# Kernel tuning notes

Hardware: AMD Instinct MI355X
Metric: run time of the kernel (lower is better)

The kernel has to match this reference:

```python
import jax, jax.numpy as jnp
import numpy as np

B = 32        # number of graphs
NPG = 2048    # nodes per graph (equal sizes -> max_size == NPG)
N = B * NPG   # total nodes
DEG = 16      # average degree
E = N * DEG   # total edges
F_IN = 128    # num_node_feats
LATENT = [32, 32, 32, 1]
TOTAL = sum(LATENT)  # 97
K = 30        # phi output size (DGCNN k)
OUT = 32      # output_dim


def setup_inputs() -> dict:
    key = jax.random.key(0)
    ks = jax.random.split(key, 16)
    node_feat = jax.random.normal(ks[0], (N, F_IN), jnp.float32)

    # edges constrained within each graph (block-diagonal n2n adjacency)
    rng = np.random.default_rng(0)
    offsets = np.repeat(np.arange(B, dtype=np.int64) * NPG, NPG * DEG)
    src = rng.integers(0, NPG, size=E) + offsets
    dst = rng.integers(0, NPG, size=E) + offsets
    edge_index = jnp.asarray(np.stack([src, dst]).astype(np.int32))

    # node_degs = in-degree + 1, shape [N, 1]
    degs = np.bincount(dst, minlength=N).astype(np.float32)
    node_degs = jnp.asarray(degs + 1.0)[:, None]

    def lin(k, fan_in, fan_out):
        s = 1.0 / np.sqrt(fan_in)
        kw, kb = jax.random.split(k)
        W = jax.random.uniform(kw, (fan_in, fan_out), jnp.float32, -s, s)
        b = jax.random.uniform(kb, (fan_out,), jnp.float32, -s, s)
        return W, b

    dims = [F_IN] + LATENT
    params = {}
    for i in range(len(LATENT)):
        W, b = lin(ks[1 + i], dims[i], dims[i + 1])
        params[f"W{i}"] = W
        params[f"b{i}"] = b
    params["phi_W"], params["phi_b"] = lin(ks[10], TOTAL, K)
    params["rho_W"], params["rho_b"] = lin(ks[11], K, OUT)

    return dict(node_feat=node_feat, node_degs=node_degs, edge_index=edge_index, **params)


def reference(node_feat, node_degs, W0, b0, W1, b1, W2, b2, W3, b3,
              phi_W, phi_b, rho_W, rho_b, edge_index):
    src, dst = edge_index[0], edge_index[1]
    n = node_feat.shape[0]

    def spmm(x):  # n2n adjacency @ x via gather + segment-sum
        return jax.ops.segment_sum(x[src], dst, num_segments=n)

    h = node_feat
    layers = [(W0, b0), (W1, b1), (W2, b2), (W3, b3)]
    cats = []
    for W, b in layers:
        pooled = spmm(h) + h                       # A h + h
        h = jnp.tanh((pooled @ W + b) / node_degs)  # linear, degree norm, tanh
        cats.append(h)
    msg = jnp.concatenate(cats, axis=1)            # [N, 97]

    # sortpooling-to-batched tensor: equal graph sizes -> pure reshape
    batched = msg.reshape(B, NPG, TOTAL)

    # DeepSets invariant model: rho(sum_i phi(x_i))
    phi = jax.nn.relu(batched @ phi_W + phi_b)     # [B, NPG, K]
    summed = jnp.sum(phi, axis=1)                  # [B, K]
    out = summed @ rho_W + rho_b                   # [B, OUT]
    return out
```

## Files before the change

### kernel.cpp

```cpp
#include <hip/hip_runtime.h>
#include <hip/hip_bf16.h>

#define NN 65536
#define NE (NN * 16)
#define NG 32
#define MAXD 64

#define WS_CURSOR 0
#define WS_SUMMED 262144
#define WS_ELL    1048576
#define WS_ZA     (WS_ELL + NN * MAXD * 4)
#define WS_ZB     (WS_ZA + NN * 32 * 4)
#define WS_H1     (WS_ZB + NN * 32 * 4)
#define WS_H2     (WS_H1 + NN * 32 * 4)
#define WS_H3     (WS_H2 + NN * 32 * 4)
#define WS_Z4     (WS_H3 + NN * 32 * 4)

__device__ __forceinline__ int xcd_swz(int b, int chunk) {
    return (b & 7) * chunk + (b >> 3);
}

__global__ __launch_bounds__(256) void k_build(const int* __restrict__ ei,
                                               int* __restrict__ cursor,
                                               int* __restrict__ ell) {
    int blk = xcd_swz(blockIdx.x, NE / 1024 / 8);
    int idx = blk * 256 + threadIdx.x;
    const int4* e4 = (const int4*)ei;
    int4 s = e4[idx];
    int4 d = e4[NE / 4 + idx];
    int t;
    t = atomicAdd(&cursor[d.x], 1); if (t < MAXD) ell[d.x * MAXD + t] = s.x;
    t = atomicAdd(&cursor[d.y], 1); if (t < MAXD) ell[d.y * MAXD + t] = s.y;
    t = atomicAdd(&cursor[d.z], 1); if (t < MAXD) ell[d.z * MAXD + t] = s.z;
    t = atomicAdd(&cursor[d.w], 1); if (t < MAXD) ell[d.w * MAXD + t] = s.w;
}

__global__ __launch_bounds__(256) void k_gemm1(const float* __restrict__ feat,
                                               const float* __restrict__ W0,
                                               float* __restrict__ z1) {
    __shared__ float wl[32 * 132];
    __shared__ float hl[64 * 132];
    int tid = threadIdx.x;
    for (int i = tid; i < 128 * 32; i += 256) {
        int k = i >> 5, c = i & 31;
        wl[c * 132 + k] = W0[i];
    }
    int base = blockIdx.x * 64;
    const float* fsrc = feat + (size_t)base * 128;
    #pragma unroll
    for (int v = 0; v < 8; ++v) {
        int flat = v * 1024 + tid * 4;
        int rr = flat >> 7, kk = flat & 127;
        *(float4*)&hl[rr * 132 + kk] = *(const float4*)&fsrc[flat];
    }
    __syncthreads();
    int cg = tid & 15, rg = tid >> 4;
    int c0 = cg * 2, r0 = rg * 4;
    float acc[4][2] = {};
    #pragma unroll 2
    for (int k = 0; k < 128; k += 4) {
        float4 wa = *(const float4*)&wl[c0 * 132 + k];
        float4 wb = *(const float4*)&wl[(c0 + 1) * 132 + k];
        #pragma unroll
        for (int rr = 0; rr < 4; ++rr) {
            float4 hv = *(const float4*)&hl[(r0 + rr) * 132 + k];
            acc[rr][0] += hv.x * wa.x + hv.y * wa.y + hv.z * wa.z + hv.w * wa.w;
            acc[rr][1] += hv.x * wb.x + hv.y * wb.y + hv.z * wb.z + hv.w * wb.w;
        }
    }
    #pragma unroll
    for (int rr = 0; rr < 4; ++rr) {
        int d = base + r0 + rr;
        z1[d * 32 + c0]     = acc[rr][0];
        z1[d * 32 + c0 + 1] = acc[rr][1];
    }
}

__device__ __forceinline__ float gather32(const int* __restrict__ row, int cnt,
                                          const float* __restrict__ zin, int c) {
    int i0 = row[c];
    float acc = 0.f;
    int m = cnt < 32 ? cnt : 32;
    int j = 0;
    for (; j + 8 <= m; j += 8) {
        int s0 = __shfl(i0, j, 32),     s1 = __shfl(i0, j + 1, 32);
        int s2 = __shfl(i0, j + 2, 32), s3 = __shfl(i0, j + 3, 32);
        int s4 = __shfl(i0, j + 4, 32), s5 = __shfl(i0, j + 5, 32);
        int s6 = __shfl(i0, j + 6, 32), s7 = __shfl(i0, j + 7, 32);
        float t0 = zin[s0 * 32 + c], t1 = zin[s1 * 32 + c];
        float t2 = zin[s2 * 32 + c], t3 = zin[s3 * 32 + c];
        float t4 = zin[s4 * 32 + c], t5 = zin[s5 * 32 + c];
        float t6 = zin[s6 * 32 + c], t7 = zin[s7 * 32 + c];
        acc += ((t0 + t1) + (t2 + t3)) + ((t4 + t5) + (t6 + t7));
    }
    for (; j + 2 <= m; j += 2) {
        int s0 = __shfl(i0, j, 32), s1 = __shfl(i0, j + 1, 32);
        float t0 = zin[s0 * 32 + c], t1 = zin[s1 * 32 + c];
        acc += t0 + t1;
    }
    for (; j < m; ++j) acc += zin[__shfl(i0, j, 32) * 32 + c];
    if (cnt > 32) {
        int i1 = row[32 + c];
        for (int j2 = 32; j2 < cnt; ++j2)
            acc += zin[__shfl(i1, j2 - 32, 32) * 32 + c];
    }
    return acc;
}

__global__ __launch_bounds__(256) void k_layer(const int* __restrict__ cursor,
                                               const int* __restrict__ ell,
                                               const float* __restrict__ zin,
                                               const float* __restrict__ degs,
                                               const float* __restrict__ bias,
                                               const float* __restrict__ Wn,
                                               float* __restrict__ hout,
                                               float* __restrict__ znext) {
    __shared__ float wt[32 * 36];
    __shared__ float hl[8][36];
    int tid = threadIdx.x;
    for (int i = tid; i < 1024; i += 256) {
        int k = i >> 5, c = i & 31;
        wt[c * 36 + k] = Wn[i];
    }
    int blk = xcd_swz(blockIdx.x, NN / 8 / 8);
    int r = tid >> 5, c = tid & 31;
    int d = blk * 8 + r;
    int cnt = cursor[d]; if (cnt > MAXD) cnt = MAXD;
    const int* row = ell + (size_t)d * MAXD;
    float acc = gather32(row, cnt, zin, c);
    float val = tanhf((acc + zin[d * 32 + c] + bias[c]) / degs[d]);
    hout[d * 32 + c] = val;
    hl[r][c] = val;
    __syncthreads();
    const float* hrow = &hl[r][0];
    const float* wrow = wt + c * 36;
    float4 a4 = {0.f, 0.f, 0.f, 0.f};
    #pragma unroll
    for (int k = 0; k < 32; k += 4) {
        float4 hv = *(const float4*)&hrow[k];
        float4 wv = *(const float4*)&wrow[k];
        a4.x += hv.x * wv.x; a4.y += hv.y * wv.y;
        a4.z += hv.z * wv.z; a4.w += hv.w * wv.w;
    }
    znext[d * 32 + c] = (a4.x + a4.y) + (a4.z + a4.w);
}

__global__ __launch_bounds__(256) void k_layer3(const int* __restrict__ cursor,
                                                const int* __restrict__ ell,
                                                const float* __restrict__ zin,
                                                const float* __restrict__ degs,
                                                const float* __restrict__ bias,
                                                const float* __restrict__ W3,
                                                float* __restrict__ hout,
                                                float* __restrict__ z4) {
    int tid = threadIdx.x;
    int blk = xcd_swz(blockIdx.x, NN / 8 / 8);
    int r = tid >> 5, c = tid & 31;
    int d = blk * 8 + r;
    int cnt = cursor[d]; if (cnt > MAXD) cnt = MAXD;
    const int* row = ell + (size_t)d * MAXD;
    float acc = gather32(row, cnt, zin, c);
    float val = tanhf((acc + zin[d * 32 + c] + bias[c]) / degs[d]);
    hout[d * 32 + c] = val;
    float v = val * W3[c];
    #pragma unroll
    for (int off = 16; off; off >>= 1) v += __shfl_xor(v, off, 32);
    if (c == 0) z4[d] = v;
}

__global__ __launch_bounds__(256) void k_phi(const int* __restrict__ cursor,
                                             const int* __restrict__ ell,
                                             const float* __restrict__ z4,
                                             const float* __restrict__ degs,
                                             const float* __restrict__ b3,
                                             const float* __restrict__ h1,
                                             const float* __restrict__ h2,
                                             const float* __restrict__ h3,
                                             const float* __restrict__ phiW,
                                             const float* __restrict__ phib,
                                             float* __restrict__ summed) {
    __shared__ float pl[30 * 100];
    __shared__ float ml[8 * 100];
    __shared__ float part[4][32];
    int tid = threadIdx.x;
    for (int i = tid; i < 30 * 97; i += 256) {
        int cc = i / 97, jj = i - cc * 97;
        pl[cc * 100 + jj] = phiW[jj * 30 + cc];
    }
    int blk = xcd_swz(blockIdx.x, NN / 8 / 8);
    int r = tid >> 5, c = tid & 31;
    int d = blk * 8 + r;
    int g = d >> 11;
    int cnt = cursor[d]; if (cnt > MAXD) cnt = MAXD;
    const int* row = ell + (size_t)d * MAXD;
    float acc = 0.f;
    for (int j = c; j < cnt; j += 32) acc += z4[row[j]];
    #pragma unroll
    for (int off = 16; off; off >>= 1) acc += __shfl_xor(acc, off, 32);
    float h4 = tanhf((acc + z4[d] + b3[0]) / degs[d]);
    ml[r * 100 + c]      = h1[d * 32 + c];
    ml[r * 100 + 32 + c] = h2[d * 32 + c];
    ml[r * 100 + 64 + c] = h3[d * 32 + c];
    if (c == 0) ml[r * 100 + 96] = h4;
    __syncthreads();
    float s = 0.f;
    if (c < 30) {
        const float* mrow = ml + r * 100;
        const float* prow = pl + c * 100;
        float4 a4 = {0.f, 0.f, 0.f, 0.f};
        #pragma unroll
        for (int j = 0; j < 96; j += 4) {
            float4 mv = *(const float4*)&mrow[j];
            float4 pv = *(const float4*)&prow[j];
            a4.x += mv.x * pv.x; a4.y += mv.y * pv.y;
            a4.z += mv.z * pv.z; a4.w += mv.w * pv.w;
        }
        s = (a4.x + a4.y) + (a4.z + a4.w) + mrow[96] * prow[96] + phib[c];
        s = fmaxf(s, 0.f);
    }
    s += __shfl_down(s, 32);
    int wave = tid >> 6;
    if ((tid & 63) < 32) part[wave][tid & 31] = s;
    __syncthreads();
    if (tid < 32) {
        float tot = part[0][tid] + part[1][tid] + part[2][tid] + part[3][tid];
        if (tid < 30) atomicAdd(&summed[g * 30 + tid], tot);
    }
}

__global__ __launch_bounds__(1024) void k_rho(const float* __restrict__ summed,
                                              const float* __restrict__ rhoW,
                                              const float* __restrict__ rhob,
                                              float* __restrict__ out) {
    int tid = threadIdx.x;
    int b = tid >> 5, o = tid & 31;
    float s = rhob[o];
    #pragma unroll
    for (int k = 0; k < 30; ++k) s += summed[b * 30 + k] * rhoW[k * 32 + o];
    out[tid] = s;
}

extern "C" void kernel_launch(void* const* d_in, const int* in_sizes, int n_in,
                              void* d_out, int out_size, void* d_ws, size_t ws_size,
                              hipStream_t stream) {
    const float* feat = (const float*)d_in[0];
    const float* degs = (const float*)d_in[1];
    const int*   ei   = (const int*)d_in[2];
    const float* W0   = (const float*)d_in[3];
    const float* b0   = (const float*)d_in[4];
    const float* W1   = (const float*)d_in[5];
    const float* b1   = (const float*)d_in[6];
    const float* W2   = (const float*)d_in[7];
    const float* b2   = (const float*)d_in[8];
    const float* W3   = (const float*)d_in[9];
    const float* b3   = (const float*)d_in[10];
    const float* phiW = (const float*)d_in[11];
    const float* phib = (const float*)d_in[12];
    const float* rhoW = (const float*)d_in[13];
    const float* rhob = (const float*)d_in[14];

    char* ws = (char*)d_ws;
    int*   cursor = (int*)(ws + WS_CURSOR);
    float* summed = (float*)(ws + WS_SUMMED);
    int*   ell    = (int*)(ws + WS_ELL);
    float* za     = (float*)(ws + WS_ZA);
    float* zb     = (float*)(ws + WS_ZB);
    float* h1     = (float*)(ws + WS_H1);
    float* h2     = (float*)(ws + WS_H2);
    float* h3     = (float*)(ws + WS_H3);
    float* z4     = (float*)(ws + WS_Z4);
    float* out    = (float*)d_out;

    hipMemsetAsync(ws, 0, WS_SUMMED + NG * 30 * 4, stream);

    k_build <<<NE / 1024, 256, 0, stream>>>(ei, cursor, ell);
    k_gemm1 <<<NN / 64, 256, 0, stream>>>(feat, W0, za);
    k_layer <<<NN / 8, 256, 0, stream>>>(cursor, ell, za, degs, b0, W1, h1, zb);
    k_layer <<<NN / 8, 256, 0, stream>>>(cursor, ell, zb, degs, b1, W2, h2, za);
    k_layer3<<<NN / 8, 256, 0, stream>>>(cursor, ell, za, degs, b2, W3, h3, z4);
    k_phi   <<<NN / 8, 256, 0, stream>>>(cursor, ell, z4, degs, b3, h1, h2, h3, phiW, phib, summed);
    k_rho   <<<1, 1024, 0, stream>>>(summed, rhoW, rhob, out);
}
```

Baseline: 263.1 us.

## Build CSR from degree scan and gather neighbours with float4 lanes

Replaces the padded ELL adjacency with a compact CSR whose row offsets come from a per-graph prefix scan of node_degs. The gather kernels now give each node 8 lanes that each load float4 slices, so one layer block covers 32 nodes. Exact tanhf and division are swapped for an exp-based tanh and a hardware reciprocal. k_phi is widened to 16 nodes per block. The aim is less wasted adjacency memory, wider vector loads and cheaper transcendentals. The cost is an extra scan kernel, and the code relies on node_degs matching the in-degree exactly, which the input data guarantees.

```diff
diff --git a/kernel.cpp b/kernel.cpp
--- a/kernel.cpp
+++ b/kernel.cpp
@@ -4,12 +4,12 @@
 #define NN 65536
 #define NE (NN * 16)
 #define NG 32
-#define MAXD 64
 
 #define WS_CURSOR 0
 #define WS_SUMMED 262144
+#define WS_ROWPTR 278528
 #define WS_ELL    1048576
-#define WS_ZA     (WS_ELL + NN * MAXD * 4)
+#define WS_ZA     (WS_ELL + NN * 64 * 4)
 #define WS_ZB     (WS_ZA + NN * 32 * 4)
 #define WS_H1     (WS_ZB + NN * 32 * 4)
 #define WS_H2     (WS_H1 + NN * 32 * 4)
@@ -20,19 +20,52 @@
     return (b & 7) * chunk + (b >> 3);
 }
 
+__device__ __forceinline__ float ftanh(float x) {
+    float xc = fmaxf(fminf(x, 15.f), -15.f);
+    float e = __expf(2.f * xc);
+    return (e - 1.f) * __builtin_amdgcn_rcpf(e + 1.f);
+}
+
+__global__ __launch_bounds__(1024) void k_scan(const float* __restrict__ degs,
+                                               int* __restrict__ rowptr) {
+    __shared__ int part[1024];
+    int g = blockIdx.x, t = threadIdx.x;
+    int base = g * 2048;
+    int c0 = (int)degs[base + 2 * t] - 1;
+    int c1 = (int)degs[base + 2 * t + 1] - 1;
+    int sum = c0 + c1;
+    part[t] = sum;
+    __syncthreads();
+    for (int off = 1; off < 1024; off <<= 1) {
+        int v = (t >= off) ? part[t - off] : 0;
+        __syncthreads();
+        part[t] += v;
+        __syncthreads();
+    }
+    int excl = part[t] - sum;
+    int gbase = g * 32768;
+    rowptr[base + 2 * t]     = gbase + excl;
+    rowptr[base + 2 * t + 1] = gbase + excl + c0;
+}
+
 __global__ __launch_bounds__(256) void k_build(const int* __restrict__ ei,
+                                               const int* __restrict__ rowptr,
                                                int* __restrict__ cursor,
-                                               int* __restrict__ ell) {
-    int blk = xcd_swz(blockIdx.x, NE / 1024 / 8);
+                                               int* __restrict__ csr) {
+    int blk = xcd_swz(blockIdx.x, 128);
     int idx = blk * 256 + threadIdx.x;
     const int4* e4 = (const int4*)ei;
     int4 s = e4[idx];
     int4 d = e4[NE / 4 + idx];
-    int t;
-    t = atomicAdd(&cursor[d.x], 1); if (t < MAXD) ell[d.x * MAXD + t] = s.x;
-    t = atomicAdd(&cursor[d.y], 1); if (t < MAXD) ell[d.y * MAXD + t] = s.y;
-    t = atomicAdd(&cursor[d.z], 1); if (t < MAXD) ell[d.z * MAXD + t] = s.z;
-    t = atomicAdd(&cursor[d.w], 1); if (t < MAXD) ell[d.w * MAXD + t] = s.w;
+    int r0 = rowptr[d.x], r1 = rowptr[d.y], r2 = rowptr[d.z], r3 = rowptr[d.w];
+    int t0 = atomicAdd(&cursor[d.x], 1);
+    int t1 = atomicAdd(&cursor[d.y], 1);
+    int t2 = atomicAdd(&cursor[d.z], 1);
+    int t3 = atomicAdd(&cursor[d.w], 1);
+    csr[r0 + t0] = s.x;
+    csr[r1 + t1] = s.y;
+    csr[r2 + t2] = s.z;
+    csr[r3 + t3] = s.w;
 }
 
 __global__ __launch_bounds__(256) void k_gemm1(const float* __restrict__ feat,
@@ -76,102 +109,138 @@
     }
 }
 
-__device__ __forceinline__ float gather32(const int* __restrict__ row, int cnt,
-                                          const float* __restrict__ zin, int c) {
-    int i0 = row[c];
-    float acc = 0.f;
+#define GB8(iv) do {                                                           \
+    int s0=__shfl((iv),0,8), s1=__shfl((iv),1,8), s2=__shfl((iv),2,8), s3=__shfl((iv),3,8); \
+    int s4=__shfl((iv),4,8), s5=__shfl((iv),5,8), s6=__shfl((iv),6,8), s7=__shfl((iv),7,8); \
+    float4 v0=*(const float4*)&zin[(size_t)s0*32+q4];                          \
+    float4 v1=*(const float4*)&zin[(size_t)s1*32+q4];                          \
+    float4 v2=*(const float4*)&zin[(size_t)s2*32+q4];                          \
+    float4 v3=*(const float4*)&zin[(size_t)s3*32+q4];                          \
+    float4 v4=*(const float4*)&zin[(size_t)s4*32+q4];                          \
+    float4 v5=*(const float4*)&zin[(size_t)s5*32+q4];                          \
+    float4 v6=*(const float4*)&zin[(size_t)s6*32+q4];                          \
+    float4 v7=*(const float4*)&zin[(size_t)s7*32+q4];                          \
+    acc.x += ((v0.x+v1.x)+(v2.x+v3.x)) + ((v4.x+v5.x)+(v6.x+v7.x));            \
+    acc.y += ((v0.y+v1.y)+(v2.y+v3.y)) + ((v4.y+v5.y)+(v6.y+v7.y));            \
+    acc.z += ((v0.z+v1.z)+(v2.z+v3.z)) + ((v4.z+v5.z)+(v6.z+v7.z));            \
+    acc.w += ((v0.w+v1.w)+(v2.w+v3.w)) + ((v4.w+v5.w)+(v6.w+v7.w));            \
+} while (0)
+
+__device__ __forceinline__ float4 gatherf4(const int* __restrict__ row, int cnt,
+                                           const float* __restrict__ zin,
+                                           int q4, float4 acc) {
+    int q = q4 >> 2;
+    int i0 = row[q], i1 = row[8 + q], i2 = row[16 + q], i3 = row[24 + q];
     int m = cnt < 32 ? cnt : 32;
-    int j = 0;
-    for (; j + 8 <= m; j += 8) {
-        int s0 = __shfl(i0, j, 32),     s1 = __shfl(i0, j + 1, 32);
-        int s2 = __shfl(i0, j + 2, 32), s3 = __shfl(i0, j + 3, 32);
-        int s4 = __shfl(i0, j + 4, 32), s5 = __shfl(i0, j + 5, 32);
-        int s6 = __shfl(i0, j + 6, 32), s7 = __shfl(i0, j + 7, 32);
-        float t0 = zin[s0 * 32 + c], t1 = zin[s1 * 32 + c];
-        float t2 = zin[s2 * 32 + c], t3 = zin[s3 * 32 + c];
-        float t4 = zin[s4 * 32 + c], t5 = zin[s5 * 32 + c];
-        float t6 = zin[s6 * 32 + c], t7 = zin[s7 * 32 + c];
-        acc += ((t0 + t1) + (t2 + t3)) + ((t4 + t5) + (t6 + t7));
-    }
-    for (; j + 2 <= m; j += 2) {
-        int s0 = __shfl(i0, j, 32), s1 = __shfl(i0, j + 1, 32);
-        float t0 = zin[s0 * 32 + c], t1 = zin[s1 * 32 + c];
-        acc += t0 + t1;
-    }
-    for (; j < m; ++j) acc += zin[__shfl(i0, j, 32) * 32 + c];
-    if (cnt > 32) {
-        int i1 = row[32 + c];
-        for (int j2 = 32; j2 < cnt; ++j2)
-            acc += zin[__shfl(i1, j2 - 32, 32) * 32 + c];
+    if (m >= 8)  GB8(i0);
+    if (m >= 16) GB8(i1);
+    if (m >= 24) GB8(i2);
+    if (m >= 32) GB8(i3);
+    int done = m & ~7;
+    if (done < m) {
+        int ivr = (done == 0) ? i0 : (done == 8) ? i1 : (done == 16) ? i2 : i3;
+        for (int j = done; j < m; ++j) {
+            int s = __shfl(ivr, j - done, 8);
+            float4 v = *(const float4*)&zin[(size_t)s * 32 + q4];
+            acc.x += v.x; acc.y += v.y; acc.z += v.z; acc.w += v.w;
+        }
+    }
+    for (int j = 32; j < cnt; ++j) {
+        int s = row[j];
+        float4 v = *(const float4*)&zin[(size_t)s * 32 + q4];
+        acc.x += v.x; acc.y += v.y; acc.z += v.z; acc.w += v.w;
     }
     return acc;
 }
 
-__global__ __launch_bounds__(256) void k_layer(const int* __restrict__ cursor,
-                                               const int* __restrict__ ell,
+__global__ __launch_bounds__(256) void k_layer(const int* __restrict__ rowptr,
+                                               const float* __restrict__ degs,
+                                               const int* __restrict__ csr,
                                                const float* __restrict__ zin,
-                                               const float* __restrict__ degs,
                                                const float* __restrict__ bias,
                                                const float* __restrict__ Wn,
                                                float* __restrict__ hout,
                                                float* __restrict__ znext) {
     __shared__ float wt[32 * 36];
-    __shared__ float hl[8][36];
+    __shared__ float hl[32 * 36];
     int tid = threadIdx.x;
     for (int i = tid; i < 1024; i += 256) {
         int k = i >> 5, c = i & 31;
         wt[c * 36 + k] = Wn[i];
     }
-    int blk = xcd_swz(blockIdx.x, NN / 8 / 8);
-    int r = tid >> 5, c = tid & 31;
-    int d = blk * 8 + r;
-    int cnt = cursor[d]; if (cnt > MAXD) cnt = MAXD;
-    const int* row = ell + (size_t)d * MAXD;
-    float acc = gather32(row, cnt, zin, c);
-    float val = tanhf((acc + zin[d * 32 + c] + bias[c]) / degs[d]);
-    hout[d * 32 + c] = val;
-    hl[r][c] = val;
-    __syncthreads();
-    const float* hrow = &hl[r][0];
-    const float* wrow = wt + c * 36;
-    float4 a4 = {0.f, 0.f, 0.f, 0.f};
-    #pragma unroll
-    for (int k = 0; k < 32; k += 4) {
-        float4 hv = *(const float4*)&hrow[k];
-        float4 wv = *(const float4*)&wrow[k];
-        a4.x += hv.x * wv.x; a4.y += hv.y * wv.y;
-        a4.z += hv.z * wv.z; a4.w += hv.w * wv.w;
-    }
-    znext[d * 32 + c] = (a4.x + a4.y) + (a4.z + a4.w);
-}
-
-__global__ __launch_bounds__(256) void k_layer3(const int* __restrict__ cursor,
-                                                const int* __restrict__ ell,
+    int blk = xcd_swz(blockIdx.x, 256);
+    int r = tid >> 3, q4 = (tid & 7) * 4;
+    int d = blk * 32 + r;
+    float degv = degs[d];
+    int cnt = (int)degv - 1;
+    const int* row = csr + rowptr[d];
+    float4 acc = *(const float4*)&zin[(size_t)d * 32 + q4];
+    acc = gatherf4(row, cnt, zin, q4, acc);
+    float4 b4 = *(const float4*)&bias[q4];
+    float rdeg = __builtin_amdgcn_rcpf(degv);
+    float4 val;
+    val.x = ftanh((acc.x + b4.x) * rdeg);
+    val.y = ftanh((acc.y + b4.y) * rdeg);
+    val.z = ftanh((acc.z + b4.z) * rdeg);
+    val.w = ftanh((acc.w + b4.w) * rdeg);
+    *(float4*)&hout[(size_t)d * 32 + q4] = val;
+    *(float4*)&hl[r * 36 + q4] = val;
+    __syncthreads();
+    #pragma unroll
+    for (int it = 0; it < 4; ++it) {
+        int wid = tid + it * 256;
+        int n = wid >> 5, c = wid & 31;
+        const float* hrow = &hl[n * 36];
+        const float* wrow = &wt[c * 36];
+        float4 a4 = {0.f, 0.f, 0.f, 0.f};
+        #pragma unroll
+        for (int k = 0; k < 32; k += 4) {
+            float4 hv = *(const float4*)&hrow[k];
+            float4 wv = *(const float4*)&wrow[k];
+            a4.x += hv.x * wv.x; a4.y += hv.y * wv.y;
+            a4.z += hv.z * wv.z; a4.w += hv.w * wv.w;
+        }
+        znext[(size_t)(blk * 32 + n) * 32 + c] = (a4.x + a4.y) + (a4.z + a4.w);
+    }
+}
+
+__global__ __launch_bounds__(256) void k_layer3(const int* __restrict__ rowptr,
+                                                const float* __restrict__ degs,
+                                                const int* __restrict__ csr,
                                                 const float* __restrict__ zin,
-                                                const float* __restrict__ degs,
                                                 const float* __restrict__ bias,
                                                 const float* __restrict__ W3,
                                                 float* __restrict__ hout,
                                                 float* __restrict__ z4) {
     int tid = threadIdx.x;
-    int blk = xcd_swz(blockIdx.x, NN / 8 / 8);
-    int r = tid >> 5, c = tid & 31;
-    int d = blk * 8 + r;
-    int cnt = cursor[d]; if (cnt > MAXD) cnt = MAXD;
-    const int* row = ell + (size_t)d * MAXD;
-    float acc = gather32(row, cnt, zin, c);
-    float val = tanhf((acc + zin[d * 32 + c] + bias[c]) / degs[d]);
-    hout[d * 32 + c] = val;
-    float v = val * W3[c];
-    #pragma unroll
-    for (int off = 16; off; off >>= 1) v += __shfl_xor(v, off, 32);
-    if (c == 0) z4[d] = v;
-}
-
-__global__ __launch_bounds__(256) void k_phi(const int* __restrict__ cursor,
-                                             const int* __restrict__ ell,
+    int blk = xcd_swz(blockIdx.x, 256);
+    int r = tid >> 3, q4 = (tid & 7) * 4;
+    int d = blk * 32 + r;
+    float degv = degs[d];
+    int cnt = (int)degv - 1;
+    const int* row = csr + rowptr[d];
+    float4 acc = *(const float4*)&zin[(size_t)d * 32 + q4];
+    acc = gatherf4(row, cnt, zin, q4, acc);
+    float4 b4 = *(const float4*)&bias[q4];
+    float rdeg = __builtin_amdgcn_rcpf(degv);
+    float4 val;
+    val.x = ftanh((acc.x + b4.x) * rdeg);
+    val.y = ftanh((acc.y + b4.y) * rdeg);
+    val.z = ftanh((acc.z + b4.z) * rdeg);
+    val.w = ftanh((acc.w + b4.w) * rdeg);
+    *(float4*)&hout[(size_t)d * 32 + q4] = val;
+    float4 w4 = *(const float4*)&W3[q4];
+    float v = (val.x * w4.x + val.y * w4.y) + (val.z * w4.z + val.w * w4.w);
+    v += __shfl_xor(v, 1, 8);
+    v += __shfl_xor(v, 2, 8);
+    v += __shfl_xor(v, 4, 8);
+    if ((tid & 7) == 0) z4[d] = v;
+}
+
+__global__ __launch_bounds__(512) void k_phi(const int* __restrict__ rowptr,
+                                             const float* __restrict__ degs,
+                                             const int* __restrict__ csr,
                                              const float* __restrict__ z4,
-                                             const float* __restrict__ degs,
                                              const float* __restrict__ b3,
                                              const float* __restrict__ h1,
                                              const float* __restrict__ h2,
@@ -180,27 +249,28 @@
                                              const float* __restrict__ phib,
                                              float* __restrict__ summed) {
     __shared__ float pl[30 * 100];
-    __shared__ float ml[8 * 100];
-    __shared__ float part[4][32];
-    int tid = threadIdx.x;
-    for (int i = tid; i < 30 * 97; i += 256) {
+    __shared__ float ml[16 * 100];
+    __shared__ float part[8][32];
+    int tid = threadIdx.x;
+    for (int i = tid; i < 30 * 97; i += 512) {
         int cc = i / 97, jj = i - cc * 97;
         pl[cc * 100 + jj] = phiW[jj * 30 + cc];
     }
-    int blk = xcd_swz(blockIdx.x, NN / 8 / 8);
+    int blk = xcd_swz(blockIdx.x, 512);
     int r = tid >> 5, c = tid & 31;
-    int d = blk * 8 + r;
+    int d = blk * 16 + r;
     int g = d >> 11;
-    int cnt = cursor[d]; if (cnt > MAXD) cnt = MAXD;
-    const int* row = ell + (size_t)d * MAXD;
+    float degv = degs[d];
+    int cnt = (int)degv - 1;
+    const int* row = csr + rowptr[d];
     float acc = 0.f;
     for (int j = c; j < cnt; j += 32) acc += z4[row[j]];
     #pragma unroll
     for (int off = 16; off; off >>= 1) acc += __shfl_xor(acc, off, 32);
-    float h4 = tanhf((acc + z4[d] + b3[0]) / degs[d]);
-    ml[r * 100 + c]      = h1[d * 32 + c];
-    ml[r * 100 + 32 + c] = h2[d * 32 + c];
-    ml[r * 100 + 64 + c] = h3[d * 32 + c];
+    float h4 = ftanh((acc + z4[d] + b3[0]) * __builtin_amdgcn_rcpf(degv));
+    ml[r * 100 + c]      = h1[(size_t)d * 32 + c];
+    ml[r * 100 + 32 + c] = h2[(size_t)d * 32 + c];
+    ml[r * 100 + 64 + c] = h3[(size_t)d * 32 + c];
     if (c == 0) ml[r * 100 + 96] = h4;
     __syncthreads();
     float s = 0.f;
@@ -223,7 +293,9 @@
     if ((tid & 63) < 32) part[wave][tid & 31] = s;
     __syncthreads();
     if (tid < 32) {
-        float tot = part[0][tid] + part[1][tid] + part[2][tid] + part[3][tid];
+        float tot = 0.f;
+        #pragma unroll
+        for (int w = 0; w < 8; ++w) tot += part[w][tid];
         if (tid < 30) atomicAdd(&summed[g * 30 + tid], tot);
     }
 }
@@ -262,7 +334,8 @@
     char* ws = (char*)d_ws;
     int*   cursor = (int*)(ws + WS_CURSOR);
     float* summed = (float*)(ws + WS_SUMMED);
-    int*   ell    = (int*)(ws + WS_ELL);
+    int*   rowptr = (int*)(ws + WS_ROWPTR);
+    int*   csr    = (int*)(ws + WS_ELL);
     float* za     = (float*)(ws + WS_ZA);
     float* zb     = (float*)(ws + WS_ZB);
     float* h1     = (float*)(ws + WS_H1);
@@ -273,11 +346,12 @@
 
     hipMemsetAsync(ws, 0, WS_SUMMED + NG * 30 * 4, stream);
 
-    k_build <<<NE / 1024, 256, 0, stream>>>(ei, cursor, ell);
+    k_scan  <<<NG, 1024, 0, stream>>>(degs, rowptr);
+    k_build <<<NE / 1024, 256, 0, stream>>>(ei, rowptr, cursor, csr);
     k_gemm1 <<<NN / 64, 256, 0, stream>>>(feat, W0, za);
-    k_layer <<<NN / 8, 256, 0, stream>>>(cursor, ell, za, degs, b0, W1, h1, zb);
-    k_layer <<<NN / 8, 256, 0, stream>>>(cursor, ell, zb, degs, b1, W2, h2, za);
-    k_layer3<<<NN / 8, 256, 0, stream>>>(cursor, ell, za, degs, b2, W3, h3, z4);
-    k_phi   <<<NN / 8, 256, 0, stream>>>(cursor, ell, z4, degs, b3, h1, h2, h3, phiW, phib, summed);
+    k_layer <<<NN / 32, 256, 0, stream>>>(rowptr, degs, csr, za, b0, W1, h1, zb);
+    k_layer <<<NN / 32, 256, 0, stream>>>(rowptr, degs, csr, zb, b1, W2, h2, za);
+    k_layer3<<<NN / 32, 256, 0, stream>>>(rowptr, degs, csr, za, b2, W3, h3, z4);
+    k_phi   <<<NN / 16, 512, 0, stream>>>(rowptr, degs, csr, z4, b3, h1, h2, h3, phiW, phib, summed);
     k_rho   <<<1, 1024, 0, stream>>>(summed, rhoW, rhob, out);
 }
```

Result: slower. 295.0 us (+12.1%).
